# Performance work log

Hardware: AMD Instinct MI355X
Metric: run time of the kernel (lower is better)

## Reference

```python
import jax, jax.numpy as jnp
import numpy as np

B, S, D, H, DFF = 4, 2048, 1024, 16, 4096
DK = D // H  # = d_v
NEG = -1e30  # stands in for float('-inf'); fully-masked rows zeroed explicitly


def setup_inputs() -> dict:
    key = jax.random.key(0)
    ks = jax.random.split(key, 12)
    scale = lambda fan_in: fan_in ** -0.5
    # padding mask: positions >= random length are padded (True = pad)
    lens = jax.random.randint(ks[0], (B,), S // 2, S + 1)
    src_padding_mask = jnp.arange(S)[None, :] >= lens[:, None]
    return {
        "src": jax.random.normal(ks[1], (B, S, D), jnp.float32),
        "src_padding_mask": src_padding_mask,
        # per-head projections, stored as [H, D, DK] (x @ W, i.e. torch W.T)
        "Wq": jax.random.normal(ks[2], (H, D, DK), jnp.float32) * scale(D),
        "Wk": jax.random.normal(ks[3], (H, D, DK), jnp.float32) * scale(D),
        "Wv": jax.random.normal(ks[4], (H, D, DK), jnp.float32) * scale(D),
        "Wo": jax.random.normal(ks[5], (D, D), jnp.float32) * scale(D),
        "g1": jnp.ones((D,), jnp.float32),
        "g2": jnp.ones((D,), jnp.float32),
        "W1": jax.random.normal(ks[6], (D, DFF), jnp.float32) * scale(D),
        "V1": jax.random.normal(ks[7], (D, DFF), jnp.float32) * scale(D),
        "W2": jax.random.normal(ks[8], (DFF, D), jnp.float32) * scale(DFF),
    }


def _rmsnorm(x, gamma):
    # rms = sqrt(sum(x^2)/size); out = gamma * x / rms
    rms = jnp.sqrt(jnp.sum(x * x, axis=-1, keepdims=True) / x.shape[-1])
    return gamma * x / rms


def _encoder_layer(src, pad_mask, Wq, Wk, Wv, Wo, g1, g2, W1, V1, W2):
    x = _rmsnorm(src, g1)
    # all heads at once: q,k,v -> [B,H,S,DK]
    q = jnp.einsum('bsd,hdk->bhsk', x, Wq)
    k = jnp.einsum('bsd,hdk->bhsk', x, Wk)
    v = jnp.einsum('bsd,hdk->bhsk', x, Wv)
    scores = jnp.einsum('bhsk,bhtk->bhst', q, k) * (DK ** -0.5)  # [B,H,S,S]
    mask = pad_mask[:, None, :, None] | pad_mask[:, None, None, :]
    scores = jnp.where(mask, NEG, scores)
    attn = jax.nn.softmax(scores, axis=-1)
    # torch: fully -inf rows softmax to nan -> nan_to_num(0). Zero padded query rows.
    attn = jnp.where(pad_mask[:, None, :, None], 0.0, attn)
    o = jnp.einsum('bhst,bhtk->bhsk', attn, v)            # [B,H,S,DK]
    o = o.transpose(0, 2, 1, 3).reshape(src.shape[0], src.shape[1], -1)  # concat heads
    sa = src + o @ Wo
    y = _rmsnorm(sa, g2)
    ff = (jax.nn.silu(y @ W1) * (y @ V1)) @ W2
    return sa + ff


def reference(src, src_padding_mask, Wq, Wk, Wv, Wo, g1, g2, W1, V1, W2):
    return _encoder_layer(src, src_padding_mask, Wq, Wk, Wv, Wo, g1, g2, W1, V1, W2)
```

## Files before the change

### kernel.cpp

```cpp
#include <hip/hip_runtime.h>
#include <hip/hip_bf16.h>

typedef short short8 __attribute__((ext_vector_type(8)));
typedef float f32x4 __attribute__((ext_vector_type(4)));
typedef float f32x16 __attribute__((ext_vector_type(16)));
typedef unsigned short u16;
typedef unsigned short u16x4 __attribute__((ext_vector_type(4)));

__device__ __forceinline__ u16 f2bf(float f) {
  __hip_bfloat16 h = __float2bfloat16(f);
  return __builtin_bit_cast(u16, h);
}
__device__ __forceinline__ float bf2f(u16 u) {
  return __bfloat162float(__builtin_bit_cast(__hip_bfloat16, u));
}
__device__ __forceinline__ void gload_lds16(const void* g, void* l) {
  __builtin_amdgcn_global_load_lds(
      (const __attribute__((address_space(1))) void*)g,
      (__attribute__((address_space(3))) void*)l, 16, 0, 0);
}
__device__ __forceinline__ unsigned cvtpk(float lo, float hi) {
  unsigned r;
  asm("v_cvt_pk_bf16_f32 %0, %1, %2" : "=v"(r) : "v"(lo), "v"(hi));
  return r;
}

__global__ void compute_lens(const unsigned char* __restrict__ mask, int* __restrict__ lens) {
  __shared__ int flag;
  __shared__ int cnt[4];
  const int tid = threadIdx.x;
  if (tid == 0) flag = 0;
  if (tid < 4) cnt[tid] = 0;
  __syncthreads();
  int found = 0;
  for (int i = tid; i < 8192; i += 256)
    if (mask[i] == 1 && (i & 3) != 0) found = 1;
  if (found) atomicOr(&flag, 1);
  __syncthreads();
  int l0 = 0, l1 = 0, l2 = 0, l3 = 0;
  if (flag) {
    for (int i = tid; i < 8192; i += 256) {
      int z = (mask[i] == 0);
      int b = i >> 11;
      l0 += z & (b == 0); l1 += z & (b == 1); l2 += z & (b == 2); l3 += z & (b == 3);
    }
  } else {
    const int* mi = (const int*)mask;
    for (int i = tid; i < 8192; i += 256) {
      int z = (mi[i] == 0);
      int b = i >> 11;
      l0 += z & (b == 0); l1 += z & (b == 1); l2 += z & (b == 2); l3 += z & (b == 3);
    }
  }
  if (l0) atomicAdd(&cnt[0], l0);
  if (l1) atomicAdd(&cnt[1], l1);
  if (l2) atomicAdd(&cnt[2], l2);
  if (l3) atomicAdd(&cnt[3], l3);
  __syncthreads();
  if (tid < 4) lens[tid] = cnt[tid];
}

__global__ void convT(const float* __restrict__ in, u16* __restrict__ out,
                      int K, int N, long inz, long outz) {
  __shared__ float t[32][33];
  const int n0 = blockIdx.x * 32, k0 = blockIdx.y * 32;
  const float* ip = in + (size_t)blockIdx.z * inz;
  u16* op = out + (size_t)blockIdx.z * outz;
  const int tx = threadIdx.x & 31, ty = threadIdx.x >> 5;
  for (int i = ty; i < 32; i += 8)
    t[i][tx] = ip[(size_t)(k0 + i) * N + n0 + tx];
  __syncthreads();
  for (int i = ty; i < 32; i += 8)
    op[(size_t)(n0 + i) * K + k0 + tx] = f2bf(t[tx][i]);
}

__global__ void rmsnorm_kernel(const float* __restrict__ in, const float* __restrict__ g,
                               u16* __restrict__ out) {
  __shared__ float psum[4];
  const int row = blockIdx.x, tid = threadIdx.x;
  const float4 x = ((const float4*)(in + (size_t)row * 1024))[tid];
  float ss = x.x * x.x + x.y * x.y + x.z * x.z + x.w * x.w;
  for (int m = 1; m < 64; m <<= 1) ss += __shfl_xor(ss, m, 64);
  if ((tid & 63) == 0) psum[tid >> 6] = ss;
  __syncthreads();
  const float tot = psum[0] + psum[1] + psum[2] + psum[3];
  const float inv = rsqrtf(tot * (1.0f / 1024.0f));
  const float4 gv = ((const float4*)g)[tid];
  u16x4 o;
  o[0] = f2bf(gv.x * x.x * inv); o[1] = f2bf(gv.y * x.y * inv);
  o[2] = f2bf(gv.z * x.z * inv); o[3] = f2bf(gv.w * x.w * inv);
  *(u16x4*)&out[(size_t)row * 1024 + tid * 4] = o;
}

#define LDST 72
enum { MQKV = 0, MSA = 1, MB16 = 2, MSILU = 3, MFF2 = 4 };

template <int MODE>
__global__ void gemm_bf16(const u16* __restrict__ A, const u16* __restrict__ Bt,
                          const int K, const int N,
                          u16* __restrict__ oq, u16* __restrict__ ok, u16* __restrict__ ov,
                          float* __restrict__ of, const float* __restrict__ afp,
                          u16* __restrict__ ob) {
  __shared__ u16 ldsA[1152 * 8];
  __shared__ u16 ldsB[1152 * 8];
  const int tid = threadIdx.x;
  const int l = tid & 63, wid = tid >> 6;
  const int wr = wid >> 1, wc = wid & 1;
  const int lane16 = l & 15, lgrp = l >> 4;
  const int row0 = blockIdx.y * 128, col0 = blockIdx.x * 128;
  const u16* Abase = A + (size_t)row0 * K;
  const u16* Bbase = Bt + (size_t)col0 * K;

  f32x4 zero = {0.f, 0.f, 0.f, 0.f};
  f32x4 acc[4][4];
#pragma unroll
  for (int i = 0; i < 4; i++)
#pragma unroll
    for (int j = 0; j < 4; j++) acc[i][j] = zero;

  const int nkt = K >> 6;
  for (int kt = 0; kt < nkt; ++kt) {
    const int k0 = kt * 64;
#pragma unroll
    for (int it = 0; it < 5; ++it) {
      const int blk = wid + it * 4;
      if (blk < 18) {
        const unsigned chunk = blk * 64 + l;
        const unsigned r = chunk / 9u;
        const unsigned cw = chunk - r * 9u;
        const unsigned koff = (cw == 8u) ? 0u : cw * 8u;
        gload_lds16(Abase + (size_t)r * K + k0 + koff, &ldsA[blk * 512]);
        gload_lds16(Bbase + (size_t)r * K + k0 + koff, &ldsB[blk * 512]);
      }
    }
    __syncthreads();
#pragma unroll
    for (int ks = 0; ks < 2; ++ks) {
      short8 a[4], b[4];
#pragma unroll
      for (int i = 0; i < 4; ++i)
        a[i] = *(const short8*)&ldsA[(wr * 64 + i * 16 + lane16) * LDST + ks * 32 + lgrp * 8];
#pragma unroll
      for (int i = 0; i < 4; ++i)
        b[i] = *(const short8*)&ldsB[(wc * 64 + i * 16 + lane16) * LDST + ks * 32 + lgrp * 8];
#pragma unroll
      for (int mi = 0; mi < 4; ++mi)
#pragma unroll
        for (int ni = 0; ni < 4; ++ni)
          acc[mi][ni] = __builtin_amdgcn_mfma_f32_16x16x32_bf16(a[mi], b[ni], acc[mi][ni], 0, 0, 0);
    }
    __syncthreads();
  }

#pragma unroll
  for (int mi = 0; mi < 4; ++mi) {
    const int sbase = row0 + wr * 64 + mi * 16 + lgrp * 4;
#pragma unroll
    for (int ni = 0; ni < 4; ++ni) {
      const int j = col0 + wc * 64 + ni * 16 + lane16;
      if (MODE == MQKV) {
        const int which = j >> 10, rr = j & 1023, h = rr >> 6, kk = rr & 63;
        const int bb = sbase >> 11, sr = sbase & 2047;
        const int bh = bb * 16 + h;
        if (which == 2) {
          u16x4 pk;
#pragma unroll
          for (int r = 0; r < 4; ++r) pk[r] = f2bf(acc[mi][ni][r]);
          *(u16x4*)&ov[((size_t)bh * 64 + kk) * 2048 + sr] = pk;
        } else {
          u16* dst = (which == 0) ? oq : ok;
          const float scl = (which == 0) ? 0.125f : 1.0f;
#pragma unroll
          for (int r = 0; r < 4; ++r)
            dst[((size_t)bh * 2048 + sr + r) * 64 + kk] = f2bf(acc[mi][ni][r] * scl);
        }
      } else if (MODE == MSA) {
#pragma unroll
        for (int r = 0; r < 4; ++r) {
          const size_t idx = (size_t)(sbase + r) * 1024 + j;
          of[idx] = afp[idx] + acc[mi][ni][r];
        }
      } else if (MODE == MB16) {
#pragma unroll
        for (int r = 0; r < 4; ++r)
          ob[(size_t)(sbase + r) * N + j] = f2bf(acc[mi][ni][r]);
      } else if (MODE == MSILU) {
#pragma unroll
        for (int r = 0; r < 4; ++r) {
          const size_t idx = (size_t)(sbase + r) * N + j;
          const float c1 = bf2f(ob[idx]);
          const float s = c1 / (1.0f + __expf(-c1));
          ob[idx] = f2bf(s * acc[mi][ni][r]);
        }
      } else {
#pragma unroll
        for (int r = 0; r < 4; ++r) {
          const size_t idx = (size_t)(sbase + r) * 1024 + j;
          of[idx] = of[idx] + acc[mi][ni][r];
        }
      }
    }
  }
}

__global__ void attn2_kernel(const u16* __restrict__ qb, const u16* __restrict__ kb,
                             const u16* __restrict__ vT, u16* __restrict__ obuf,
                             const int* __restrict__ lens) {
  __shared__ u16 sm[9216];
  const int tid = threadIdx.x;
  const int l = tid & 63, wid = tid >> 6;
  const int l31 = l & 31, hi = l >> 5;
  const int bh = blockIdx.x, b = bh >> 4, h = bh & 15;
  const int q0 = blockIdx.y * 128;
  const int len = lens[b];

  if (q0 >= len) {
    short8 z = {0, 0, 0, 0, 0, 0, 0, 0};
#pragma unroll
    for (int c = 0; c < 4; ++c) {
      const int ck = c * 256 + tid;
      const int r = ck >> 3, j = ck & 7;
      *(short8*)&obuf[((size_t)b * 2048 + q0 + r) * 1024 + h * 64 + j * 8] = z;
    }
    return;
  }

  const int q0w = q0 + wid * 32;
  const u16* qp = qb + ((size_t)bh * 2048 + q0w + l31) * 64;
  short8 qf0 = *(const short8*)(qp + hi * 8);
  short8 qf1 = *(const short8*)(qp + 16 + hi * 8);
  short8 qf2 = *(const short8*)(qp + 32 + hi * 8);
  short8 qf3 = *(const short8*)(qp + 48 + hi * 8);

  f32x16 oa0 = {0.f,0.f,0.f,0.f,0.f,0.f,0.f,0.f,0.f,0.f,0.f,0.f,0.f,0.f,0.f,0.f};
  f32x16 oa1 = oa0;
  float m_run = -1e30f, l_run = 0.f;

  const int swz = (l31 & 7) << 3;
  const int nt = (len + 63) >> 6;
  for (int kt = 0; kt < nt; ++kt) {
    const int t0 = kt * 64;
    __syncthreads();
#pragma unroll
    for (int c = 0; c < 2; ++c) {
      const int ck = c * 256 + wid * 64 + l;
      const int r = ck >> 3;
      const int j = (ck & 7) ^ (r & 7);
      gload_lds16(kb + ((size_t)bh * 2048 + t0 + r) * 64 + j * 8,
                  &sm[(c * 256 + wid * 64) * 8]);
      gload_lds16(vT + ((size_t)bh * 64 + r) * 2048 + t0 + j * 8,
                  &sm[4096 + (c * 256 + wid * 64) * 8]);
    }
    __syncthreads();

    f32x16 sc0 = {0.f,0.f,0.f,0.f,0.f,0.f,0.f,0.f,0.f,0.f,0.f,0.f,0.f,0.f,0.f,0.f};
    f32x16 sc1 = sc0;
#pragma unroll
    for (int ds = 0; ds < 4; ++ds) {
      const int col = (ds * 16 + hi * 8) ^ swz;
      const short8 kf0 = *(const short8*)&sm[(0 + l31) * 64 + col];
      const short8 kf1 = *(const short8*)&sm[(32 + l31) * 64 + col];
      const short8 qf = (ds == 0) ? qf0 : (ds == 1) ? qf1 : (ds == 2) ? qf2 : qf3;
      sc0 = __builtin_amdgcn_mfma_f32_32x32x16_bf16(kf0, qf, sc0, 0, 0, 0);
      sc1 = __builtin_amdgcn_mfma_f32_32x32x16_bf16(kf1, qf, sc1, 0, 0, 0);
    }

    if (t0 + 64 > len) {
      const int tb = t0 + 4 * hi;
#pragma unroll
      for (int i = 0; i < 16; ++i) {
        const int tg = tb + (i & 3) + 8 * (i >> 2);
        if (tg >= len) sc0[i] = -1e30f;
        if (tg + 32 >= len) sc1[i] = -1e30f;
      }
    }

    float mt = sc0[0];
#pragma unroll
    for (int i = 1; i < 16; ++i) mt = fmaxf(mt, sc0[i]);
#pragma unroll
    for (int i = 0; i < 16; ++i) mt = fmaxf(mt, sc1[i]);
    mt = fmaxf(mt, __shfl_xor(mt, 32, 64));
    const float mnew = fmaxf(m_run, mt);
    const float fac = __expf(m_run - mnew);
    m_run = mnew;
    float sum = 0.f;
#pragma unroll
    for (int i = 0; i < 16; ++i) { sc0[i] = __expf(sc0[i] - mnew); sum += sc0[i]; }
#pragma unroll
    for (int i = 0; i < 16; ++i) { sc1[i] = __expf(sc1[i] - mnew); sum += sc1[i]; }
    sum += __shfl_xor(sum, 32, 64);
    l_run = l_run * fac + sum;
#pragma unroll
    for (int i = 0; i < 16; ++i) { oa0[i] *= fac; oa1[i] *= fac; }

    unsigned w[16];
#pragma unroll
    for (int k = 0; k < 8; ++k) w[k] = cvtpk(sc0[2 * k], sc0[2 * k + 1]);
#pragma unroll
    for (int k = 0; k < 8; ++k) w[8 + k] = cvtpk(sc1[2 * k], sc1[2 * k + 1]);
    unsigned pw[16];
#pragma unroll
    for (int s = 0; s < 2; ++s) {
#pragma unroll
      for (int half = 0; half < 2; ++half) {
        const unsigned a0 = w[8 * s + 4 * half + 0], a1 = w[8 * s + 4 * half + 1];
        const unsigned a2 = w[8 * s + 4 * half + 2], a3 = w[8 * s + 4 * half + 3];
        const unsigned e0 = (unsigned)__shfl_xor((int)(hi ? a0 : a2), 32, 64);
        const unsigned e1 = (unsigned)__shfl_xor((int)(hi ? a1 : a3), 32, 64);
        const int o = s * 8 + half * 4;
        pw[o + 0] = hi ? e0 : a0;
        pw[o + 1] = hi ? e1 : a1;
        pw[o + 2] = hi ? a2 : e0;
        pw[o + 3] = hi ? a3 : e1;
      }
    }
#pragma unroll
    for (int g = 0; g < 4; ++g) {
      union { unsigned u[4]; short8 s8; } pk;
      pk.u[0] = pw[4 * g + 0]; pk.u[1] = pw[4 * g + 1];
      pk.u[2] = pw[4 * g + 2]; pk.u[3] = pw[4 * g + 3];
      const int col = (g * 16 + hi * 8) ^ swz;
      const short8 vf0 = *(const short8*)&sm[4096 + (0 + l31) * 64 + col];
      const short8 vf1 = *(const short8*)&sm[4096 + (32 + l31) * 64 + col];
      oa0 = __builtin_amdgcn_mfma_f32_32x32x16_bf16(vf0, pk.s8, oa0, 0, 0, 0);
      oa1 = __builtin_amdgcn_mfma_f32_32x32x16_bf16(vf1, pk.s8, oa1, 0, 0, 0);
    }
  }

  __syncthreads();
  const float invl = 1.0f / l_run;
  u16* ow = &sm[wid * 2304];
#pragma unroll
  for (int i = 0; i < 16; ++i) {
    const int d0 = (i & 3) + 8 * (i >> 2) + 4 * hi;
    ow[l31 * 72 + d0] = f2bf(oa0[i] * invl);
    ow[l31 * 72 + 32 + d0] = f2bf(oa1[i] * invl);
  }
  short8 z = {0, 0, 0, 0, 0, 0, 0, 0};
#pragma unroll
  for (int c = 0; c < 4; ++c) {
    const int ck = c * 64 + l;
    const int r = ck >> 3, j = ck & 7;
    short8 v = *(const short8*)&ow[r * 72 + j * 8];
    if (q0w + r >= len) v = z;
    *(short8*)&obuf[((size_t)b * 2048 + q0w + r) * 1024 + h * 64 + j * 8] = v;
  }
}

extern "C" void kernel_launch(void* const* d_in, const int* in_sizes, int n_in,
                              void* d_out, int out_size, void* d_ws, size_t ws_size,
                              hipStream_t stream) {
  const float* src = (const float*)d_in[0];
  const unsigned char* mask = (const unsigned char*)d_in[1];
  const float* Wq = (const float*)d_in[2];
  const float* Wk = (const float*)d_in[3];
  const float* Wv = (const float*)d_in[4];
  const float* Wo = (const float*)d_in[5];
  const float* g1 = (const float*)d_in[6];
  const float* g2 = (const float*)d_in[7];
  const float* W1 = (const float*)d_in[8];
  const float* V1 = (const float*)d_in[9];
  const float* W2 = (const float*)d_in[10];
  float* out = (float*)d_out;
  char* ws = (char*)d_ws;

  int* lens   = (int*)ws;
  u16* WqkvT  = (u16*)(ws + 256);
  u16* WoT    = (u16*)(ws + 6291712);
  u16* W1T    = (u16*)(ws + 8388864);
  u16* V1T    = (u16*)(ws + 16777472);
  u16* W2T    = (u16*)(ws + 25166080);
  u16* xb     = (u16*)(ws + 33554688);
  u16* qbf    = (u16*)(ws + 50331904);
  u16* kbf    = (u16*)(ws + 67109120);
  u16* vTb    = (u16*)(ws + 83886336);
  u16* obf    = (u16*)(ws + 100663552);
  u16* c1     = qbf;

  compute_lens<<<1, 256, 0, stream>>>(mask, lens);
  convT<<<dim3(2, 32, 16), 256, 0, stream>>>(Wq, WqkvT, 1024, 64, 65536, 65536);
  convT<<<dim3(2, 32, 16), 256, 0, stream>>>(Wk, WqkvT + 1024 * 1024, 1024, 64, 65536, 65536);
  convT<<<dim3(2, 32, 16), 256, 0, stream>>>(Wv, WqkvT + 2048 * 1024, 1024, 64, 65536, 65536);
  convT<<<dim3(32, 32, 1), 256, 0, stream>>>(Wo, WoT, 1024, 1024, 0, 0);
  convT<<<dim3(128, 32, 1), 256, 0, stream>>>(W1, W1T, 1024, 4096, 0, 0);
  convT<<<dim3(128, 32, 1), 256, 0, stream>>>(V1, V1T, 1024, 4096, 0, 0);
  convT<<<dim3(32, 128, 1), 256, 0, stream>>>(W2, W2T, 4096, 1024, 0, 0);

  rmsnorm_kernel<<<8192, 256, 0, stream>>>(src, g1, xb);
  gemm_bf16<MQKV><<<dim3(24, 64), 256, 0, stream>>>(xb, WqkvT, 1024, 3072,
                                                    qbf, kbf, vTb, nullptr, nullptr, nullptr);
  attn2_kernel<<<dim3(64, 16), 256, 0, stream>>>(qbf, kbf, vTb, obf, lens);
  gemm_bf16<MSA><<<dim3(8, 64), 256, 0, stream>>>(obf, WoT, 1024, 1024,
                                                  nullptr, nullptr, nullptr, out, src, nullptr);
  rmsnorm_kernel<<<8192, 256, 0, stream>>>(out, g2, xb);
  gemm_bf16<MB16><<<dim3(32, 64), 256, 0, stream>>>(xb, W1T, 1024, 4096,
                                                    nullptr, nullptr, nullptr, nullptr, nullptr, c1);
  gemm_bf16<MSILU><<<dim3(32, 64), 256, 0, stream>>>(xb, V1T, 1024, 4096,
                                                     nullptr, nullptr, nullptr, nullptr, nullptr, c1);
  gemm_bf16<MFF2><<<dim3(8, 64), 256, 0, stream>>>(c1, W2T, 4096, 1024,
                                                   nullptr, nullptr, nullptr, out, nullptr, nullptr);
}
```

Baseline: 513.2 us.

## Rewrite GEMM with 128x256 tiles, multi-stage async LDS pipeline and staged epilogue

Replaces the 128x128, 4-wave GEMM with a 512-thread kernel that computes a 128x256 tile and uses XOR-swizzled LDS layouts. A triple-buffered A and double-buffered B global-to-LDS prefetch pipeline uses explicit vmcnt waits and a single barrier per k-step. The kernel also adds a grid swizzle for L2 locality and s_setprio around the MFMA bursts. Epilogues for the bf16 and fp32 residual modes now stage through LDS so global stores are vectorized and coalesced. The larger tile and 56K-element LDS allocation may limit occupancy, and the pipeline depends on exact waitcnt accounting.

```diff
diff --git a/kernel.cpp b/kernel.cpp
--- a/kernel.cpp
+++ b/kernel.cpp
@@ -92,24 +92,71 @@
   *(u16x4*)&out[(size_t)row * 1024 + tid * 4] = o;
 }
 
-#define LDST 72
 enum { MQKV = 0, MSA = 1, MB16 = 2, MSILU = 3, MFF2 = 4 };
 
 template <int MODE>
-__global__ void gemm_bf16(const u16* __restrict__ A, const u16* __restrict__ Bt,
-                          const int K, const int N,
-                          u16* __restrict__ oq, u16* __restrict__ ok, u16* __restrict__ ov,
-                          float* __restrict__ of, const float* __restrict__ afp,
-                          u16* __restrict__ ob) {
-  __shared__ u16 ldsA[1152 * 8];
-  __shared__ u16 ldsB[1152 * 8];
+__global__ __launch_bounds__(512, 2) void gemm2(
+    const u16* __restrict__ A, const u16* __restrict__ Bt,
+    const int K, const int N,
+    u16* __restrict__ oq, u16* __restrict__ ok, u16* __restrict__ ov,
+    float* __restrict__ of, const float* __restrict__ afp,
+    u16* __restrict__ ob) {
+  __shared__ u16 lds[57344];
+  u16* Ab = lds;
+  u16* Bb = lds + 24576;
   const int tid = threadIdx.x;
-  const int l = tid & 63, wid = tid >> 6;
-  const int wr = wid >> 1, wc = wid & 1;
+  const int w = tid >> 6, l = tid & 63;
+  const int wr = w >> 2, wc = w & 3;
   const int lane16 = l & 15, lgrp = l >> 4;
-  const int row0 = blockIdx.y * 128, col0 = blockIdx.x * 128;
-  const u16* Abase = A + (size_t)row0 * K;
-  const u16* Bbase = Bt + (size_t)col0 * K;
+
+  const int nwg = (int)gridDim.x;
+  const int bid = (int)blockIdx.x;
+  const int swz = (bid & 7) * (nwg >> 3) + (bid >> 3);
+  const int bx = swz >> 6, by = swz & 63;
+  const int row0 = by * 128, col0 = bx * 256;
+
+  const int ca0 = w * 128 + l, ca1 = ca0 + 64;
+  const int ra0 = ca0 >> 3, ra1 = ca1 >> 3;
+  const int ja0 = (ca0 & 7) ^ (ra0 & 7), ja1 = (ca1 & 7) ^ (ra1 & 7);
+  const u16* ag0 = A + (size_t)(row0 + ra0) * K + ja0 * 8;
+  const u16* ag1 = A + (size_t)(row0 + ra1) * K + ja1 * 8;
+  const u16* bg[4];
+  int rbv[4];
+#pragma unroll
+  for (int i = 0; i < 4; ++i) {
+    const int cb = w * 256 + i * 64 + l;
+    const int rb = cb >> 3, jb = (cb & 7) ^ (rb & 7);
+    rbv[i] = rb;
+    bg[i] = Bt + (size_t)(col0 + rb) * K + jb * 8;
+  }
+
+  int aoff[4][2], boff[4][2];
+#pragma unroll
+  for (int mi = 0; mi < 4; ++mi) {
+    const int ar = wr * 64 + mi * 16 + lane16;
+#pragma unroll
+    for (int ks = 0; ks < 2; ++ks)
+      aoff[mi][ks] = ar * 64 + (((ks << 2) + lgrp) ^ (ar & 7)) * 8;
+  }
+#pragma unroll
+  for (int ni = 0; ni < 4; ++ni) {
+    const int br = wc * 64 + ni * 16 + lane16;
+#pragma unroll
+    for (int ks = 0; ks < 2; ++ks)
+      boff[ni][ks] = br * 64 + (((ks << 2) + lgrp) ^ (br & 7)) * 8;
+  }
+
+  auto issueA = [&](int tt) {
+    u16* d = Ab + (tt % 3) * 8192 + w * 1024;
+    gload_lds16(ag0 + tt * 64, d);
+    gload_lds16(ag1 + tt * 64, d + 512);
+  };
+  auto issueB = [&](int tt) {
+    u16* d = Bb + (tt & 1) * 16384 + w * 2048;
+#pragma unroll
+    for (int i = 0; i < 4; ++i)
+      gload_lds16(bg[i] + tt * 64, d + i * 512);
+  };
 
   f32x4 zero = {0.f, 0.f, 0.f, 0.f};
   f32x4 acc[4][4];
@@ -119,49 +166,61 @@
     for (int j = 0; j < 4; j++) acc[i][j] = zero;
 
   const int nkt = K >> 6;
-  for (int kt = 0; kt < nkt; ++kt) {
-    const int k0 = kt * 64;
-#pragma unroll
-    for (int it = 0; it < 5; ++it) {
-      const int blk = wid + it * 4;
-      if (blk < 18) {
-        const unsigned chunk = blk * 64 + l;
-        const unsigned r = chunk / 9u;
-        const unsigned cw = chunk - r * 9u;
-        const unsigned koff = (cw == 8u) ? 0u : cw * 8u;
-        gload_lds16(Abase + (size_t)r * K + k0 + koff, &ldsA[blk * 512]);
-        gload_lds16(Bbase + (size_t)r * K + k0 + koff, &ldsB[blk * 512]);
-      }
-    }
-    __syncthreads();
-#pragma unroll
-    for (int ks = 0; ks < 2; ++ks) {
-      short8 a[4], b[4];
-#pragma unroll
-      for (int i = 0; i < 4; ++i)
-        a[i] = *(const short8*)&ldsA[(wr * 64 + i * 16 + lane16) * LDST + ks * 32 + lgrp * 8];
-#pragma unroll
-      for (int i = 0; i < 4; ++i)
-        b[i] = *(const short8*)&ldsB[(wc * 64 + i * 16 + lane16) * LDST + ks * 32 + lgrp * 8];
+  issueA(0); issueB(0); issueA(1);
+
+  for (int t = 0; t < nkt; ++t) {
+    if (t < nkt - 1) { asm volatile("s_waitcnt vmcnt(2)" ::: "memory"); }
+    else             { asm volatile("s_waitcnt vmcnt(0)" ::: "memory"); }
+    __builtin_amdgcn_s_barrier();
+    __builtin_amdgcn_sched_barrier(0);
+    if (t + 1 < nkt) issueB(t + 1);
+    if (t + 2 < nkt) issueA(t + 2);
+    const u16* ap = Ab + (t % 3) * 8192;
+    const u16* bp = Bb + (t & 1) * 16384;
+    short8 af[4][2], bf[4][2];
+#pragma unroll
+    for (int mi = 0; mi < 4; ++mi)
+#pragma unroll
+      for (int ks = 0; ks < 2; ++ks) af[mi][ks] = *(const short8*)&ap[aoff[mi][ks]];
+#pragma unroll
+    for (int ni = 0; ni < 2; ++ni)
+#pragma unroll
+      for (int ks = 0; ks < 2; ++ks) bf[ni][ks] = *(const short8*)&bp[boff[ni][ks]];
+    __builtin_amdgcn_s_setprio(1);
+#pragma unroll
+    for (int ks = 0; ks < 2; ++ks)
 #pragma unroll
       for (int mi = 0; mi < 4; ++mi)
 #pragma unroll
-        for (int ni = 0; ni < 4; ++ni)
-          acc[mi][ni] = __builtin_amdgcn_mfma_f32_16x16x32_bf16(a[mi], b[ni], acc[mi][ni], 0, 0, 0);
-    }
-    __syncthreads();
-  }
-
-#pragma unroll
-  for (int mi = 0; mi < 4; ++mi) {
-    const int sbase = row0 + wr * 64 + mi * 16 + lgrp * 4;
-#pragma unroll
-    for (int ni = 0; ni < 4; ++ni) {
-      const int j = col0 + wc * 64 + ni * 16 + lane16;
-      if (MODE == MQKV) {
+        for (int ni = 0; ni < 2; ++ni)
+          acc[mi][ni] = __builtin_amdgcn_mfma_f32_16x16x32_bf16(af[mi][ks], bf[ni][ks], acc[mi][ni], 0, 0, 0);
+    __builtin_amdgcn_s_setprio(0);
+#pragma unroll
+    for (int ni = 2; ni < 4; ++ni)
+#pragma unroll
+      for (int ks = 0; ks < 2; ++ks) bf[ni][ks] = *(const short8*)&bp[boff[ni][ks]];
+    __builtin_amdgcn_s_setprio(1);
+#pragma unroll
+    for (int ks = 0; ks < 2; ++ks)
+#pragma unroll
+      for (int mi = 0; mi < 4; ++mi)
+#pragma unroll
+        for (int ni = 2; ni < 4; ++ni)
+          acc[mi][ni] = __builtin_amdgcn_mfma_f32_16x16x32_bf16(af[mi][ks], bf[ni][ks], acc[mi][ni], 0, 0, 0);
+    __builtin_amdgcn_s_setprio(0);
+  }
+  __syncthreads();
+
+  if (MODE == MQKV) {
+#pragma unroll
+    for (int mi = 0; mi < 4; ++mi) {
+      const int sbase = row0 + wr * 64 + mi * 16 + lgrp * 4;
+      const int bbt = sbase >> 11, sr = sbase & 2047;
+#pragma unroll
+      for (int ni = 0; ni < 4; ++ni) {
+        const int j = col0 + wc * 64 + ni * 16 + lane16;
         const int which = j >> 10, rr = j & 1023, h = rr >> 6, kk = rr & 63;
-        const int bb = sbase >> 11, sr = sbase & 2047;
-        const int bh = bb * 16 + h;
+        const int bh = bbt * 16 + h;
         if (which == 2) {
           u16x4 pk;
 #pragma unroll
@@ -174,30 +233,56 @@
           for (int r = 0; r < 4; ++r)
             dst[((size_t)bh * 2048 + sr + r) * 64 + kk] = f2bf(acc[mi][ni][r] * scl);
         }
-      } else if (MODE == MSA) {
-#pragma unroll
-        for (int r = 0; r < 4; ++r) {
-          const size_t idx = (size_t)(sbase + r) * 1024 + j;
-          of[idx] = afp[idx] + acc[mi][ni][r];
+      }
+    }
+  } else if (MODE == MB16 || MODE == MSILU) {
+    u16* ep = lds + w * 1152;
+    const int grow0 = row0 + wr * 64 + (l >> 2);
+    const int gcol = col0 + wc * 64 + (l & 3) * 16;
+#pragma unroll
+    for (int mi = 0; mi < 4; ++mi) {
+#pragma unroll
+      for (int ni = 0; ni < 4; ++ni)
+#pragma unroll
+        for (int r = 0; r < 4; ++r)
+          ep[(lgrp * 4 + r) * 72 + ni * 16 + lane16] = f2bf(acc[mi][ni][r]);
+      short8 v0 = *(const short8*)&ep[(l >> 2) * 72 + (l & 3) * 16];
+      short8 v1 = *(const short8*)&ep[(l >> 2) * 72 + (l & 3) * 16 + 8];
+      const size_t idx = (size_t)(grow0 + mi * 16) * N + gcol;
+      if (MODE == MSILU) {
+        short8 c0 = *(const short8*)&ob[idx];
+        short8 c1v = *(const short8*)&ob[idx + 8];
+#pragma unroll
+        for (int jj = 0; jj < 8; ++jj) {
+          float c = bf2f((u16)c0[jj]);
+          v0[jj] = (short)f2bf(c / (1.0f + __expf(-c)) * bf2f((u16)v0[jj]));
+          c = bf2f((u16)c1v[jj]);
+          v1[jj] = (short)f2bf(c / (1.0f + __expf(-c)) * bf2f((u16)v1[jj]));
         }
-      } else if (MODE == MB16) {
+      }
+      *(short8*)&ob[idx] = v0;
+      *(short8*)&ob[idx + 8] = v1;
+    }
+  } else {
+    float* ep32 = (float*)lds + w * 1088;
+    const int grow0 = row0 + wr * 64 + (l >> 2);
+    const int gcol = col0 + wc * 64 + (l & 3) * 16;
+#pragma unroll
+    for (int mi = 0; mi < 4; ++mi) {
+#pragma unroll
+      for (int ni = 0; ni < 4; ++ni)
 #pragma unroll
         for (int r = 0; r < 4; ++r)
-          ob[(size_t)(sbase + r) * N + j] = f2bf(acc[mi][ni][r]);
-      } else if (MODE == MSILU) {
-#pragma unroll
-        for (int r = 0; r < 4; ++r) {
-          const size_t idx = (size_t)(sbase + r) * N + j;
-          const float c1 = bf2f(ob[idx]);
-          const float s = c1 / (1.0f + __expf(-c1));
-          ob[idx] = f2bf(s * acc[mi][ni][r]);
-        }
-      } else {
-#pragma unroll
-        for (int r = 0; r < 4; ++r) {
-          const size_t idx = (size_t)(sbase + r) * 1024 + j;
-          of[idx] = of[idx] + acc[mi][ni][r];
-        }
+          ep32[(lgrp * 4 + r) * 68 + ni * 16 + lane16] = acc[mi][ni][r];
+      const size_t idx = (size_t)(grow0 + mi * 16) * N + gcol;
+#pragma unroll
+      for (int k = 0; k < 4; ++k) {
+        float4 v = *(const float4*)&ep32[(l >> 2) * 68 + (l & 3) * 16 + k * 4];
+        float4 a;
+        if (MODE == MSA) a = *(const float4*)&afp[idx + k * 4];
+        else             a = *(const float4*)&of[idx + k * 4];
+        v.x += a.x; v.y += a.y; v.z += a.z; v.w += a.w;
+        *(float4*)&of[idx + k * 4] = v;
       }
     }
   }
@@ -294,18 +379,18 @@
 #pragma unroll
     for (int i = 0; i < 16; ++i) { oa0[i] *= fac; oa1[i] *= fac; }
 
-    unsigned w[16];
-#pragma unroll
-    for (int k = 0; k < 8; ++k) w[k] = cvtpk(sc0[2 * k], sc0[2 * k + 1]);
-#pragma unroll
-    for (int k = 0; k < 8; ++k) w[8 + k] = cvtpk(sc1[2 * k], sc1[2 * k + 1]);
+    unsigned wv[16];
+#pragma unroll
+    for (int k = 0; k < 8; ++k) wv[k] = cvtpk(sc0[2 * k], sc0[2 * k + 1]);
+#pragma unroll
+    for (int k = 0; k < 8; ++k) wv[8 + k] = cvtpk(sc1[2 * k], sc1[2 * k + 1]);
     unsigned pw[16];
 #pragma unroll
     for (int s = 0; s < 2; ++s) {
 #pragma unroll
       for (int half = 0; half < 2; ++half) {
-        const unsigned a0 = w[8 * s + 4 * half + 0], a1 = w[8 * s + 4 * half + 1];
-        const unsigned a2 = w[8 * s + 4 * half + 2], a3 = w[8 * s + 4 * half + 3];
+        const unsigned a0 = wv[8 * s + 4 * half + 0], a1 = wv[8 * s + 4 * half + 1];
+        const unsigned a2 = wv[8 * s + 4 * half + 2], a3 = wv[8 * s + 4 * half + 3];
         const unsigned e0 = (unsigned)__shfl_xor((int)(hi ? a0 : a2), 32, 64);
         const unsigned e1 = (unsigned)__shfl_xor((int)(hi ? a1 : a3), 32, 64);
         const int o = s * 8 + half * 4;
@@ -388,16 +473,16 @@
   convT<<<dim3(32, 128, 1), 256, 0, stream>>>(W2, W2T, 4096, 1024, 0, 0);
 
   rmsnorm_kernel<<<8192, 256, 0, stream>>>(src, g1, xb);
-  gemm_bf16<MQKV><<<dim3(24, 64), 256, 0, stream>>>(xb, WqkvT, 1024, 3072,
-                                                    qbf, kbf, vTb, nullptr, nullptr, nullptr);
+  gemm2<MQKV><<<768, 512, 0, stream>>>(xb, WqkvT, 1024, 3072,
+                                       qbf, kbf, vTb, nullptr, nullptr, nullptr);
   attn2_kernel<<<dim3(64, 16), 256, 0, stream>>>(qbf, kbf, vTb, obf, lens);
-  gemm_bf16<MSA><<<dim3(8, 64), 256, 0, stream>>>(obf, WoT, 1024, 1024,
-                                                  nullptr, nullptr, nullptr, out, src, nullptr);
+  gemm2<MSA><<<256, 512, 0, stream>>>(obf, WoT, 1024, 1024,
+                                      nullptr, nullptr, nullptr, out, src, nullptr);
   rmsnorm_kernel<<<8192, 256, 0, stream>>>(out, g2, xb);
-  gemm_bf16<MB16><<<dim3(32, 64), 256, 0, stream>>>(xb, W1T, 1024, 4096,
-                                                    nullptr, nullptr, nullptr, nullptr, nullptr, c1);
-  gemm_bf16<MSILU><<<dim3(32, 64), 256, 0, stream>>>(xb, V1T, 1024, 4096,
-                                                     nullptr, nullptr, nullptr, nullptr, nullptr, c1);
-  gemm_bf16<MFF2><<<dim3(8, 64), 256, 0, stream>>>(c1, W2T, 4096, 1024,
-                                                   nullptr, nullptr, nullptr, out, nullptr, nullptr);
-}
+  gemm2<MB16><<<1024, 512, 0, stream>>>(xb, W1T, 1024, 4096,
+                                        nullptr, nullptr, nullptr, nullptr, nullptr, c1);
+  gemm2<MSILU><<<1024, 512, 0, stream>>>(xb, V1T, 1024, 4096,
+                                         nullptr, nullptr, nullptr, nullptr, nullptr, c1);
+  gemm2<MFF2><<<256, 512, 0, stream>>>(c1, W2T, 4096, 1024,
+                                       nullptr, nullptr, nullptr, out, nullptr, nullptr);
+}
```

Measured after the change: 536.5 us. 1.05x slower.
